# Kernel optimization log

Measured on AMD Instinct MI355X. Metric: run time of the kernel, lower is better.

The kernel has to match this reference:

```python
import jax, jax.numpy as jnp
import numpy as np

N = 8192        # nodes (A.shape[0])
D_IN = 128      # input_dim
D_OUT = 128     # output_dim
D_THETA = 256   # hardcoded in GCN_liner_theta_1
DROP_KEEP = 0.8 # DropEdge percent


def setup_inputs() -> dict:
    key = jax.random.key(0)
    ks = jax.random.split(key, 6)
    H = jax.random.normal(ks[0], (N, D_IN), dtype=jnp.float32)
    U = jax.random.uniform(ks[1], (N, N), dtype=jnp.float32)
    upper = jnp.triu((U < 0.01).astype(jnp.float32), 1)
    A_adj = upper + upper.T + jnp.eye(N, dtype=jnp.float32)
    bn_gamma = jnp.ones((D_IN,), jnp.float32)
    bn_beta = jnp.zeros((D_IN,), jnp.float32)
    W_theta = jax.random.normal(ks[2], (D_THETA, D_IN), jnp.float32) * 0.05
    b_theta = jnp.zeros((D_THETA,), jnp.float32)
    W_out = jax.random.normal(ks[3], (D_OUT, D_IN), jnp.float32) * 0.05
    b_out = jnp.zeros((D_OUT,), jnp.float32)
    return {"H": H, "A_adj": A_adj, "bn_gamma": bn_gamma, "bn_beta": bn_beta,
            "W_theta": W_theta, "b_theta": b_theta, "W_out": W_out, "b_out": b_out}


def reference(H, A_adj, bn_gamma, bn_beta, W_theta, b_theta, W_out, b_out):
    n = H.shape[0]
    # BatchNorm1d in training mode: batch stats over the node dimension
    mean = H.mean(axis=0)
    var = H.var(axis=0)  # biased, matches torch training normalization
    Hn = (H - mean) * jax.lax.rsqrt(var + 1e-5) * bn_gamma + bn_beta

    # theta projection -> pairwise euclidean distances
    Hx = Hn @ W_theta.T + b_theta                     # [N, 256]
    sq = jnp.sum(Hx * Hx, axis=1)                     # [N]
    dist = sq[:, None] + sq[None, :] - 2.0 * (Hx @ Hx.T)
    dist = jnp.sqrt(jnp.clip(dist, 1e-12, None))      # [N, N]

    A = jnp.exp(-0.2 * dist)
    A = jnp.clip(jax.nn.sigmoid(A), 0.1, None)
    # DropEdge detaches A in the original (A never carries grad)
    A = jax.lax.stop_gradient(A)

    dkey = jax.random.key(42)
    keep = jax.random.uniform(dkey, (n, n)) < DROP_KEEP
    triu = jnp.triu(jnp.ones((n, n), dtype=bool), 0)
    Bt = jnp.where(triu & keep, A, 0.0)
    B = Bt + Bt.T - jnp.diag(jnp.diag(Bt))

    mask = jnp.ceil(A_adj * 1e-5)
    A2 = B * mask + jnp.eye(n, dtype=B.dtype)
    A3 = jnp.where(A2 > 0.6, A2, 0.0)                 # threshold (host loop in torch)

    # symmetric normalization D^-1/2 A D^-1/2 without dense diag matmuls
    d_inv_sqrt = jax.lax.rsqrt(A3.sum(axis=1))        # diag always >= 1
    A_hat = A3 * d_inv_sqrt[:, None] * d_inv_sqrt[None, :]

    out = A_hat @ (Hn @ W_out.T + b_out)              # [N, D_OUT]
    out = jnp.where(out >= 0, out, 0.01 * out)        # LeakyReLU(0.01)
    return out, A3
```

## Files before the change

### kernel.cpp

```cpp
#include <hip/hip_runtime.h>
#include <cstdint>
#include <cstddef>

#define N 8192
#define DIN 128
#define DTH 256
#define DOUT 128
#define ROWCAP 256
#define LISTCAP 256

typedef float vfloat4 __attribute__((ext_vector_type(4)));

__device__ __forceinline__ void threefry_0_42(uint32_t x0, uint32_t x1,
                                              uint32_t& o0, uint32_t& o1) {
  const uint32_t ks0 = 0u;
  const uint32_t ks1 = 42u;
  const uint32_t ks2 = 0x1BD11BDAu ^ 0u ^ 42u;
  x0 += ks0; x1 += ks1;
#define TF_R(r) { x0 += x1; x1 = (x1 << (r)) | (x1 >> (32 - (r))); x1 ^= x0; }
  TF_R(13) TF_R(15) TF_R(26) TF_R(6)
  x0 += ks1; x1 += ks2 + 1u;
  TF_R(17) TF_R(29) TF_R(16) TF_R(24)
  x0 += ks2; x1 += ks0 + 2u;
  TF_R(13) TF_R(15) TF_R(26) TF_R(6)
  x0 += ks0; x1 += ks1 + 3u;
  TF_R(17) TF_R(29) TF_R(16) TF_R(24)
  x0 += ks1; x1 += ks2 + 4u;
  TF_R(13) TF_R(15) TF_R(26) TF_R(6)
  x0 += ks2; x1 += ks0 + 5u;
#undef TF_R
  o0 = x0; o1 = x1;
}

__device__ __forceinline__ bool dropedge_keep(uint32_t t) {
  uint32_t y0, y1;
  threefry_0_42(0u, t, y0, y1);
  uint32_t bits = y0 ^ y1;
  float u = __uint_as_float((bits >> 9) | 0x3f800000u) - 1.0f;
  return u < 0.8f;
}

__device__ __forceinline__ unsigned short f2bf(float v) {
  uint32_t u = __float_as_uint(v);
  u += 0x7fffu + ((u >> 16) & 1u);
  return (unsigned short)(u >> 16);
}

__global__ __launch_bounds__(256) void k_pre(
    const float* __restrict__ H,
    const float* __restrict__ Wt, const float* __restrict__ bt,
    const float* __restrict__ Wo, const float* __restrict__ bo,
    float* __restrict__ part_s, float* __restrict__ part_s2,
    float* __restrict__ Wc, float* __restrict__ bc,
    float* __restrict__ deg ) {
  int b = blockIdx.x;
  int tid = threadIdx.x;
  if (b < 64) {
    __shared__ float ls[8][DIN];
    __shared__ float ls2[8][DIN];
    int rg = tid >> 5;
    int c4 = tid & 31;
    int rbase = b * 128;
    float s[4] = {0,0,0,0}, s2[4] = {0,0,0,0};
    for (int k = 0; k < 16; ++k) {
      int r = rbase + rg + k * 8;
      float4 h = ((const float4*)(H + (size_t)r * DIN))[c4];
      s[0] += h.x; s2[0] += h.x * h.x;
      s[1] += h.y; s2[1] += h.y * h.y;
      s[2] += h.z; s2[2] += h.z * h.z;
      s[3] += h.w; s2[3] += h.w * h.w;
    }
#pragma unroll
    for (int q = 0; q < 4; ++q) { ls[rg][c4*4+q] = s[q]; ls2[rg][c4*4+q] = s2[q]; }
    __syncthreads();
    if (tid < DIN) {
      float a = 0.f, bb = 0.f;
#pragma unroll
      for (int g = 0; g < 8; ++g) { a += ls[g][tid]; bb += ls2[g][tid]; }
      part_s[b * DIN + tid] = a;
      part_s2[b * DIN + tid] = bb;
    }
  } else if (b < 256) {
    int idx = (b - 64) * 256 + tid;
    int k = idx / 384, c = idx % 384;
    Wc[idx] = (c < 256) ? Wt[(size_t)c * DIN + k] : Wo[(size_t)(c - 256) * DIN + k];
  } else if (b < 258) {
    int c = (b - 256) * 256 + tid;
    if (c < 384) bc[c] = (c < 256) ? bt[c] : bo[c - 256];
  } else {
    int g = (b - 258) * 256 + tid;
    ((int4*)deg)[g] = make_int4(0, 0, 0, 0);
  }
}

__global__ __launch_bounds__(256) void k_rows(
    const float* __restrict__ H,
    const float* __restrict__ part_s, const float* __restrict__ part_s2,
    const float* __restrict__ gamma, const float* __restrict__ beta,
    const float* __restrict__ Wc, const float* __restrict__ bc,
    unsigned short* __restrict__ Hxh, float* __restrict__ HW,
    float* __restrict__ sq, float* __restrict__ A3) {
  int tid = threadIdx.x;
  int b = blockIdx.x;
  if (b >= 512) {
    vfloat4* row = (vfloat4*)(A3 + (size_t)(b - 512) * N);
    const vfloat4 z = {0.f, 0.f, 0.f, 0.f};
#pragma unroll
    for (int it = 0; it < 8; ++it)
      __builtin_nontemporal_store(z, row + tid + it * 256);
    return;
  }
  __shared__ __align__(16) float ssc[DIN];
  __shared__ __align__(16) float ssh[DIN];
  __shared__ float hn[16][DIN];
  if (tid < DIN) {
    float s = 0.f, s2 = 0.f;
    for (int g = 0; g < 64; ++g) { s += part_s[g*DIN+tid]; s2 += part_s2[g*DIN+tid]; }
    float mean = s * (1.0f / N);
    float var  = s2 * (1.0f / N) - mean * mean;
    float sc = rsqrtf(var + 1e-5f) * gamma[tid];
    ssc[tid] = sc;
    ssh[tid] = beta[tid] - mean * sc;
  }
  __syncthreads();
  int base = b * 16;
#pragma unroll
  for (int k = 0; k < 2; ++k) {
    int f = tid + k * 256;
    int r = f >> 5, c4 = f & 31;
    float4 h  = ((const float4*)(H + (size_t)(base + r) * DIN))[c4];
    float4 sc = ((const float4*)ssc)[c4];
    float4 sh = ((const float4*)ssh)[c4];
    h.x = h.x * sc.x + sh.x; h.y = h.y * sc.y + sh.y;
    h.z = h.z * sc.z + sh.z; h.w = h.w * sc.w + sh.w;
    ((float4*)hn[r])[c4] = h;
  }
  __syncthreads();
  int w = tid >> 6, lane = tid & 63;
  int r0 = w * 4;
  float acc[4][6];
#pragma unroll
  for (int r = 0; r < 4; ++r)
#pragma unroll
    for (int q = 0; q < 6; ++q) acc[r][q] = 0.f;

  for (int k4 = 0; k4 < 32; ++k4) {
    float4 h[4];
#pragma unroll
    for (int r = 0; r < 4; ++r) h[r] = ((const float4*)hn[r0 + r])[k4];
#pragma unroll
    for (int kk = 0; kk < 4; ++kk) {
      const float* wrow = Wc + (size_t)(k4 * 4 + kk) * 384 + lane;
      float wv[6];
#pragma unroll
      for (int q = 0; q < 6; ++q) wv[q] = wrow[64 * q];
#pragma unroll
      for (int r = 0; r < 4; ++r) {
        float hs = (kk == 0) ? h[r].x : (kk == 1) ? h[r].y
                 : (kk == 2) ? h[r].z : h[r].w;
#pragma unroll
        for (int q = 0; q < 6; ++q) acc[r][q] += hs * wv[q];
      }
    }
  }
#pragma unroll
  for (int r = 0; r < 4; ++r) {
    int row = base + r0 + r;
    float s = 0.f;
#pragma unroll
    for (int q = 0; q < 4; ++q) {
      float v = acc[r][q] + bc[lane + 64 * q];
      Hxh[(size_t)row * DTH + lane + 64 * q] = f2bf(v);
      s += v * v;
    }
#pragma unroll
    for (int off = 32; off > 0; off >>= 1) s += __shfl_xor(s, off, 64);
    if (lane == 0) sq[row] = s;
#pragma unroll
    for (int q = 4; q < 6; ++q) {
      float v = acc[r][q] + bc[lane + 64 * q];
      HW[(size_t)row * DOUT + lane + 64 * (q - 4)] = v;
    }
  }
}

__global__ __launch_bounds__(256) void k_main(
    const float* __restrict__ A_adj, const unsigned short* __restrict__ Hxh,
    const float* __restrict__ sq, float* __restrict__ A3,
    float* __restrict__ deg, int* __restrict__ nnz_cnt,
    int* __restrict__ nnz_idx, float* __restrict__ nnz_val) {
  int i = blockIdx.x;
  int tid = threadIdx.x;
  __shared__ float4 hx4[64];
  __shared__ int   s_list[LISTCAP];
  __shared__ int   s_cnt;
  if (tid == 0) s_cnt = 0;
  ((float*)hx4)[tid] = __uint_as_float(((uint32_t)Hxh[(size_t)i * DTH + tid]) << 16);
  __syncthreads();

  const vfloat4* arow = (const vfloat4*)(A_adj + (size_t)i * N);
  int q0 = i >> 2;
  for (int q4 = q0 + tid; q4 < N / 4; q4 += 256) {
    vfloat4 a = __builtin_nontemporal_load(arow + q4);
    int jb = q4 * 4;
    float av[4] = {a.x, a.y, a.z, a.w};
#pragma unroll
    for (int q = 0; q < 4; ++q) {
      int j = jb + q;
      if (av[q] != 0.f && j >= i) {
        int p = atomicAdd(&s_cnt, 1);
        if (p < LISTCAP) s_list[p] = j;
      }
    }
  }
  __syncthreads();

  int M = min(s_cnt, LISTCAP);
  float sqi = sq[i];
  for (int t = tid; t < M; t += 256) {
    int j = s_list[t];
    bool keep = dropedge_keep((uint32_t)i * (uint32_t)N + (uint32_t)j);
    float dist;
    if (j == i) {
      dist = 1e-6f;
    } else {
      const uint4* hj = (const uint4*)(Hxh + (size_t)j * DTH);
      float dot = 0.f;
#pragma unroll 8
      for (int c = 0; c < 32; ++c) {
        uint4 u = hj[c];
        float4 f0 = hx4[2 * c], f1 = hx4[2 * c + 1];
        dot += __uint_as_float(u.x << 16) * f0.x
             + __uint_as_float(u.x & 0xffff0000u) * f0.y
             + __uint_as_float(u.y << 16) * f0.z
             + __uint_as_float(u.y & 0xffff0000u) * f0.w
             + __uint_as_float(u.z << 16) * f1.x
             + __uint_as_float(u.z & 0xffff0000u) * f1.y
             + __uint_as_float(u.w << 16) * f1.z
             + __uint_as_float(u.w & 0xffff0000u) * f1.w;
      }
      dist = sqrtf(fmaxf(sqi + sq[j] - 2.0f * dot, 1e-12f));
    }
    float aval = expf(-0.2f * dist);
    float sg = fmaxf(1.0f / (1.0f + expf(-aval)), 0.1f);
    float bb = keep ? sg : 0.0f;
    float a2 = bb + ((i == j) ? 1.0f : 0.0f);
    float a3v = (a2 > 0.6f) ? a2 : 0.0f;
    if (a3v != 0.f) {
      A3[(size_t)i * N + j] = a3v;
      atomicAdd(&deg[i], a3v);
      int p = atomicAdd(&nnz_cnt[i], 1);
      if (p < ROWCAP) {
        nnz_idx[(size_t)i * ROWCAP + p] = j;
        nnz_val[(size_t)i * ROWCAP + p] = a3v;
      }
      if (j != i) {
        A3[(size_t)j * N + i] = a3v;
        atomicAdd(&deg[j], a3v);
        int p2 = atomicAdd(&nnz_cnt[j], 1);
        if (p2 < ROWCAP) {
          nnz_idx[(size_t)j * ROWCAP + p2] = i;
          nnz_val[(size_t)j * ROWCAP + p2] = a3v;
        }
      }
    }
  }
}

__global__ __launch_bounds__(128) void k_post(
    const float* __restrict__ HW, const float* __restrict__ deg,
    const int* __restrict__ nnz_cnt, const int* __restrict__ nnz_idx,
    const float* __restrict__ nnz_val, float* __restrict__ out) {
  int i = blockIdx.x;
  int c = threadIdx.x;
  int cnt = min(nnz_cnt[i], ROWCAP);
  float acc = 0.f;
  for (int e = 0; e < cnt; ++e) {
    int j = nnz_idx[(size_t)i * ROWCAP + e];
    float v = nnz_val[(size_t)i * ROWCAP + e];
    acc += v * rsqrtf(deg[j]) * HW[(size_t)j * DOUT + c];
  }
  float o = rsqrtf(deg[i]) * acc;
  out[(size_t)i * DOUT + c] = (o >= 0.f) ? o : 0.01f * o;
}

extern "C" void kernel_launch(void* const* d_in, const int* in_sizes, int n_in,
                              void* d_out, int out_size, void* d_ws, size_t ws_size,
                              hipStream_t stream) {
  const float* H     = (const float*)d_in[0];
  const float* A_adj = (const float*)d_in[1];
  const float* gamma = (const float*)d_in[2];
  const float* beta  = (const float*)d_in[3];
  const float* Wt    = (const float*)d_in[4];
  const float* bt    = (const float*)d_in[5];
  const float* Wo    = (const float*)d_in[6];
  const float* bo    = (const float*)d_in[7];

  float* out = (float*)d_out;
  float* A3  = out + (size_t)N * DOUT;

  float* ws    = (float*)d_ws;
  unsigned short* Hxh = (unsigned short*)ws;
  float* sq    = ws + (size_t)N * 128;
  float* HW    = sq + N;
  float* deg   = HW + (size_t)N * DOUT;
  int*   nnz_cnt = (int*)(deg + N);
  int*   nnz_idx = nnz_cnt + N;
  float* nnz_val = (float*)(nnz_idx + (size_t)N * ROWCAP);
  float* part_s  = nnz_val + (size_t)N * ROWCAP;
  float* part_s2 = part_s + 64 * DIN;
  float* Wc      = part_s2 + 64 * DIN;
  float* bc      = Wc + 128 * 384;

  k_pre<<<274, 256, 0, stream>>>(H, Wt, bt, Wo, bo, part_s, part_s2, Wc, bc, deg);
  k_rows<<<512 + N, 256, 0, stream>>>(H, part_s, part_s2, gamma, beta, Wc, bc,
                                      Hxh, HW, sq, A3);
  k_main<<<N, 256, 0, stream>>>(A_adj, Hxh, sq, A3, deg, nnz_cnt, nnz_idx, nnz_val);
  k_post<<<N, DOUT, 0, stream>>>(HW, deg, nnz_cnt, nnz_idx, nnz_val, out);
}
```

Before: 459.9 us.

## Build a global edge list during adjacency scan and compute edges in parallel

The adjacency scan moves into the row-projection kernel, where blocks alternate between zeroing A3 (four rows at a time, with the diagonal written directly) and collecting upper-triangular edges into a global packed edge list. A new edge-parallel kernel gives each edge to eight lanes, which compute the bf16 dot product together and reduce with shuffles. This replaces the per-row kernel, whose per-row workload was unbalanced and which used one thread per dot product. The post kernel now handles the diagonal term separately and processes more rows per block. The cost is a global atomic edge counter, a large edge buffer, and a dependency between the fused scan and the projection running in the same launch.

```diff
diff --git a/kernel.cpp b/kernel.cpp
--- a/kernel.cpp
+++ b/kernel.cpp
@@ -7,7 +7,8 @@
 #define DTH 256
 #define DOUT 128
 #define ROWCAP 256
-#define LISTCAP 256
+#define SCANCAP 1024
+#define EDGECAP 2000000
 
 typedef float vfloat4 __attribute__((ext_vector_type(4)));
 
@@ -44,6 +45,14 @@
   uint32_t u = __float_as_uint(v);
   u += 0x7fffu + ((u >> 16) & 1u);
   return (unsigned short)(u >> 16);
+}
+
+__device__ __forceinline__ float diag_a3(int r) {
+  bool keep = dropedge_keep((uint32_t)r * (uint32_t)N + (uint32_t)r);
+  float aval = expf(-0.2f * 1e-6f);
+  float sg = fmaxf(1.0f / (1.0f + expf(-aval)), 0.1f);
+  float bb = keep ? sg : 0.0f;
+  return bb + 1.0f;
 }
 
 __global__ __launch_bounds__(256) void k_pre(
@@ -89,27 +98,80 @@
     if (c < 384) bc[c] = (c < 256) ? bt[c] : bo[c - 256];
   } else {
     int g = (b - 258) * 256 + tid;
-    ((int4*)deg)[g] = make_int4(0, 0, 0, 0);
-  }
-}
-
-__global__ __launch_bounds__(256) void k_rows(
-    const float* __restrict__ H,
+    if (g < 4097) ((int4*)deg)[g] = make_int4(0, 0, 0, 0);
+  }
+}
+
+__global__ __launch_bounds__(256) void k_fused(
+    const float* __restrict__ H, const float* __restrict__ A_adj,
     const float* __restrict__ part_s, const float* __restrict__ part_s2,
     const float* __restrict__ gamma, const float* __restrict__ beta,
     const float* __restrict__ Wc, const float* __restrict__ bc,
     unsigned short* __restrict__ Hxh, float* __restrict__ HW,
-    float* __restrict__ sq, float* __restrict__ A3) {
+    float* __restrict__ sq, float* __restrict__ A3,
+    float* __restrict__ deg, int* __restrict__ edges,
+    int* __restrict__ edge_cnt) {
+  int b = blockIdx.x;
   int tid = threadIdx.x;
-  int b = blockIdx.x;
+
   if (b >= 512) {
-    vfloat4* row = (vfloat4*)(A3 + (size_t)(b - 512) * N);
-    const vfloat4 z = {0.f, 0.f, 0.f, 0.f};
-#pragma unroll
-    for (int it = 0; it < 8; ++it)
-      __builtin_nontemporal_store(z, row + tid + it * 256);
+    int s = b - 512;
+    if ((s & 1) == 0) {
+      int z = s >> 1;
+      int rbase = z * 4;
+      vfloat4* p = (vfloat4*)(A3 + (size_t)rbase * N);
+      const vfloat4 zv = {0.f, 0.f, 0.f, 0.f};
+#pragma unroll
+      for (int it = 0; it < 32; ++it)
+        __builtin_nontemporal_store(zv, p + tid + it * 256);
+      __syncthreads();
+      if (tid < 4) {
+        int r = rbase + tid;
+        float d = diag_a3(r);
+        A3[(size_t)r * N + r] = d;
+        deg[r] = d;
+      }
+    } else {
+      int sb = s >> 1;
+      __shared__ int s_edges[SCANCAP];
+      __shared__ int s_cnt;
+      __shared__ int s_base;
+      if (tid == 0) s_cnt = 0;
+      __syncthreads();
+      for (int rr = 0; rr < 4; ++rr) {
+        int r = sb * 4 + rr;
+        const vfloat4* arow = (const vfloat4*)(A_adj + (size_t)r * N);
+        int q0 = r >> 2;
+        for (int q4 = q0 + tid; q4 < N / 4; q4 += 256) {
+          vfloat4 a = __builtin_nontemporal_load(arow + q4);
+          int jb = q4 * 4;
+          float av[4] = {a.x, a.y, a.z, a.w};
+#pragma unroll
+          for (int q = 0; q < 4; ++q) {
+            int j = jb + q;
+            if (av[q] != 0.f && j > r) {
+              int pk = (r << 13) | j;
+              int p = atomicAdd(&s_cnt, 1);
+              if (p < SCANCAP) s_edges[p] = pk;
+              else {
+                int gp = atomicAdd(edge_cnt, 1);
+                if (gp < EDGECAP) edges[gp] = pk;
+              }
+            }
+          }
+        }
+      }
+      __syncthreads();
+      int m = min(s_cnt, SCANCAP);
+      if (tid == 0) s_base = atomicAdd(edge_cnt, m);
+      __syncthreads();
+      int base = s_base;
+      for (int t = tid; t < m; t += 256)
+        if (base + t < EDGECAP) edges[base + t] = s_edges[t];
+    }
     return;
   }
+
   __shared__ __align__(16) float ssc[DIN];
   __shared__ __align__(16) float ssh[DIN];
   __shared__ float hn[16][DIN];
@@ -184,79 +246,55 @@
   }
 }
 
-__global__ __launch_bounds__(256) void k_main(
-    const float* __restrict__ A_adj, const unsigned short* __restrict__ Hxh,
-    const float* __restrict__ sq, float* __restrict__ A3,
-    float* __restrict__ deg, int* __restrict__ nnz_cnt,
-    int* __restrict__ nnz_idx, float* __restrict__ nnz_val) {
-  int i = blockIdx.x;
-  int tid = threadIdx.x;
-  __shared__ float4 hx4[64];
-  __shared__ int   s_list[LISTCAP];
-  __shared__ int   s_cnt;
-  if (tid == 0) s_cnt = 0;
-  ((float*)hx4)[tid] = __uint_as_float(((uint32_t)Hxh[(size_t)i * DTH + tid]) << 16);
-  __syncthreads();
-
-  const vfloat4* arow = (const vfloat4*)(A_adj + (size_t)i * N);
-  int q0 = i >> 2;
-  for (int q4 = q0 + tid; q4 < N / 4; q4 += 256) {
-    vfloat4 a = __builtin_nontemporal_load(arow + q4);
-    int jb = q4 * 4;
-    float av[4] = {a.x, a.y, a.z, a.w};
-#pragma unroll
-    for (int q = 0; q < 4; ++q) {
-      int j = jb + q;
-      if (av[q] != 0.f && j >= i) {
-        int p = atomicAdd(&s_cnt, 1);
-        if (p < LISTCAP) s_list[p] = j;
-      }
-    }
-  }
-  __syncthreads();
-
-  int M = min(s_cnt, LISTCAP);
-  float sqi = sq[i];
-  for (int t = tid; t < M; t += 256) {
-    int j = s_list[t];
-    bool keep = dropedge_keep((uint32_t)i * (uint32_t)N + (uint32_t)j);
-    float dist;
-    if (j == i) {
-      dist = 1e-6f;
-    } else {
-      const uint4* hj = (const uint4*)(Hxh + (size_t)j * DTH);
-      float dot = 0.f;
-#pragma unroll 8
-      for (int c = 0; c < 32; ++c) {
-        uint4 u = hj[c];
-        float4 f0 = hx4[2 * c], f1 = hx4[2 * c + 1];
-        dot += __uint_as_float(u.x << 16) * f0.x
-             + __uint_as_float(u.x & 0xffff0000u) * f0.y
-             + __uint_as_float(u.y << 16) * f0.z
-             + __uint_as_float(u.y & 0xffff0000u) * f0.w
-             + __uint_as_float(u.z << 16) * f1.x
-             + __uint_as_float(u.z & 0xffff0000u) * f1.y
-             + __uint_as_float(u.w << 16) * f1.z
-             + __uint_as_float(u.w & 0xffff0000u) * f1.w;
-      }
-      dist = sqrtf(fmaxf(sqi + sq[j] - 2.0f * dot, 1e-12f));
-    }
-    float aval = expf(-0.2f * dist);
-    float sg = fmaxf(1.0f / (1.0f + expf(-aval)), 0.1f);
-    float bb = keep ? sg : 0.0f;
-    float a2 = bb + ((i == j) ? 1.0f : 0.0f);
-    float a3v = (a2 > 0.6f) ? a2 : 0.0f;
-    if (a3v != 0.f) {
-      A3[(size_t)i * N + j] = a3v;
-      atomicAdd(&deg[i], a3v);
-      int p = atomicAdd(&nnz_cnt[i], 1);
-      if (p < ROWCAP) {
-        nnz_idx[(size_t)i * ROWCAP + p] = j;
-        nnz_val[(size_t)i * ROWCAP + p] = a3v;
-      }
-      if (j != i) {
+__global__ __launch_bounds__(256) void k_dot(
+    const unsigned short* __restrict__ Hxh, const float* __restrict__ sq,
+    const int* __restrict__ edges, const int* __restrict__ edge_cnt,
+    float* __restrict__ A3, float* __restrict__ deg,
+    int* __restrict__ nnz_cnt, int* __restrict__ nnz_idx,
+    float* __restrict__ nnz_val) {
+  int cnt = min(*(volatile const int*)edge_cnt, EDGECAP);
+  int l = threadIdx.x & 7;
+  int g = (blockIdx.x << 5) | (threadIdx.x >> 3);
+  int stride = gridDim.x << 5;
+  for (int e = g; e < cnt; e += stride) {
+    uint32_t pk = (uint32_t)edges[e];
+    int i = pk >> 13, j = pk & 8191;
+    const uint4* hi = (const uint4*)(Hxh + (size_t)i * DTH);
+    const uint4* hj = (const uint4*)(Hxh + (size_t)j * DTH);
+    float dot = 0.f;
+#pragma unroll
+    for (int t = 0; t < 4; ++t) {
+      uint4 u = hi[t * 8 + l];
+      uint4 v = hj[t * 8 + l];
+      dot += __uint_as_float(u.x << 16)         * __uint_as_float(v.x << 16)
+           + __uint_as_float(u.x & 0xffff0000u) * __uint_as_float(v.x & 0xffff0000u)
+           + __uint_as_float(u.y << 16)         * __uint_as_float(v.y << 16)
+           + __uint_as_float(u.y & 0xffff0000u) * __uint_as_float(v.y & 0xffff0000u)
+           + __uint_as_float(u.z << 16)         * __uint_as_float(v.z << 16)
+           + __uint_as_float(u.z & 0xffff0000u) * __uint_as_float(v.z & 0xffff0000u)
+           + __uint_as_float(u.w << 16)         * __uint_as_float(v.w << 16)
+           + __uint_as_float(u.w & 0xffff0000u) * __uint_as_float(v.w & 0xffff0000u);
+    }
+    dot += __shfl_xor(dot, 1, 8);
+    dot += __shfl_xor(dot, 2, 8);
+    dot += __shfl_xor(dot, 4, 8);
+    if (l == 0) {
+      float dist = sqrtf(fmaxf(sq[i] + sq[j] - 2.0f * dot, 1e-12f));
+      bool keep = dropedge_keep((uint32_t)i * (uint32_t)N + (uint32_t)j);
+      float aval = expf(-0.2f * dist);
+      float sg = fmaxf(1.0f / (1.0f + expf(-aval)), 0.1f);
+      float a2 = keep ? sg : 0.0f;
+      float a3v = (a2 > 0.6f) ? a2 : 0.0f;
+      if (a3v != 0.f) {
+        A3[(size_t)i * N + j] = a3v;
         A3[(size_t)j * N + i] = a3v;
+        atomicAdd(&deg[i], a3v);
         atomicAdd(&deg[j], a3v);
+        int p = atomicAdd(&nnz_cnt[i], 1);
+        if (p < ROWCAP) {
+          nnz_idx[(size_t)i * ROWCAP + p] = j;
+          nnz_val[(size_t)i * ROWCAP + p] = a3v;
+        }
         int p2 = atomicAdd(&nnz_cnt[j], 1);
         if (p2 < ROWCAP) {
           nnz_idx[(size_t)j * ROWCAP + p2] = i;
@@ -267,21 +305,27 @@
   }
 }
 
-__global__ __launch_bounds__(128) void k_post(
+__global__ __launch_bounds__(256) void k_post(
     const float* __restrict__ HW, const float* __restrict__ deg,
     const int* __restrict__ nnz_cnt, const int* __restrict__ nnz_idx,
-    const float* __restrict__ nnz_val, float* __restrict__ out) {
-  int i = blockIdx.x;
-  int c = threadIdx.x;
-  int cnt = min(nnz_cnt[i], ROWCAP);
-  float acc = 0.f;
-  for (int e = 0; e < cnt; ++e) {
-    int j = nnz_idx[(size_t)i * ROWCAP + e];
-    float v = nnz_val[(size_t)i * ROWCAP + e];
-    acc += v * rsqrtf(deg[j]) * HW[(size_t)j * DOUT + c];
-  }
-  float o = rsqrtf(deg[i]) * acc;
-  out[(size_t)i * DOUT + c] = (o >= 0.f) ? o : 0.01f * o;
+    const float* __restrict__ nnz_val, const float* __restrict__ A3,
+    float* __restrict__ out) {
+  int g = threadIdx.x >> 7;
+  int c = threadIdx.x & 127;
+#pragma unroll
+  for (int k = 0; k < 2; ++k) {
+    int i = blockIdx.x * 4 + g * 2 + k;
+    float ri = rsqrtf(deg[i]);
+    float acc = A3[(size_t)i * N + i] * ri * HW[(size_t)i * DOUT + c];
+    int cnt = min(nnz_cnt[i], ROWCAP);
+    for (int e = 0; e < cnt; ++e) {
+      int j = nnz_idx[(size_t)i * ROWCAP + e];
+      float v = nnz_val[(size_t)i * ROWCAP + e];
+      acc += v * rsqrtf(deg[j]) * HW[(size_t)j * DOUT + c];
+    }
+    float o = ri * acc;
+    out[(size_t)i * DOUT + c] = (o >= 0.f) ? o : 0.01f * o;
+  }
 }
 
 extern "C" void kernel_launch(void* const* d_in, const int* in_sizes, int n_in,
@@ -304,17 +348,20 @@
   float* sq    = ws + (size_t)N * 128;
   float* HW    = sq + N;
   float* deg   = HW + (size_t)N * DOUT;
-  int*   nnz_cnt = (int*)(deg + N);
-  int*   nnz_idx = nnz_cnt + N;
-  float* nnz_val = (float*)(nnz_idx + (size_t)N * ROWCAP);
-  float* part_s  = nnz_val + (size_t)N * ROWCAP;
-  float* part_s2 = part_s + 64 * DIN;
-  float* Wc      = part_s2 + 64 * DIN;
-  float* bc      = Wc + 128 * 384;
-
-  k_pre<<<274, 256, 0, stream>>>(H, Wt, bt, Wo, bo, part_s, part_s2, Wc, bc, deg);
-  k_rows<<<512 + N, 256, 0, stream>>>(H, part_s, part_s2, gamma, beta, Wc, bc,
-                                      Hxh, HW, sq, A3);
-  k_main<<<N, 256, 0, stream>>>(A_adj, Hxh, sq, A3, deg, nnz_cnt, nnz_idx, nnz_val);
-  k_post<<<N, DOUT, 0, stream>>>(HW, deg, nnz_cnt, nnz_idx, nnz_val, out);
-}
+  int*   nnz_cnt  = (int*)(deg + N);
+  int*   edge_cnt = nnz_cnt + N;
+  int*   nnz_idx  = edge_cnt + 4;
+  float* nnz_val  = (float*)(nnz_idx + (size_t)N * ROWCAP);
+  float* part_s   = nnz_val + (size_t)N * ROWCAP;
+  float* part_s2  = part_s + 64 * DIN;
+  float* Wc       = part_s2 + 64 * DIN;
+  float* bc       = Wc + 128 * 384;
+  int*   edges    = (int*)(bc + 384);
+
+  k_pre<<<275, 256, 0, stream>>>(H, Wt, bt, Wo, bo, part_s, part_s2, Wc, bc, deg);
+  k_fused<<<4608, 256, 0, stream>>>(H, A_adj, part_s, part_s2, gamma, beta, Wc, bc,
+                                    Hxh, HW, sq, A3, deg, edges, edge_cnt);
+  k_dot<<<2048, 256, 0, stream>>>(Hxh, sq, edges, edge_cnt, A3, deg,
+                                  nnz_cnt, nnz_idx, nnz_val);
+  k_post<<<N / 4, 256, 0, stream>>>(HW, deg, nnz_cnt, nnz_idx, nnz_val, A3, out);
+}
```

New measurement: 477.6 us. +3.9%, slower.
